# Kernel optimization log

Measured on AMD Instinct MI355X. Metric: run time of the kernel, lower is better.

The kernel has to match this reference:

```python
import jax, jax.numpy as jnp
import numpy as np

B, T, V, E, H, D = 2, 2048, 32000, 1024, 16, 64


def setup_inputs() -> dict:
    key = jax.random.key(0)
    ks = jax.random.split(key, 8)
    s = 0.02  # init scale
    return {
        "X": jax.random.randint(ks[0], (B, T), 0, V),
        "tok_emb": jax.random.normal(ks[1], (V, E), jnp.float32) * s,
        "pos_emb": jax.random.normal(ks[2], (T, E), jnp.float32) * s,
        "Wq": jax.random.normal(ks[3], (H, E, D), jnp.float32) * s,
        "Wk": jax.random.normal(ks[4], (H, E, D), jnp.float32) * s,
        "Wv": jax.random.normal(ks[5], (H, E, D), jnp.float32) * s,
        "lm_W": jax.random.normal(ks[6], (E, V), jnp.float32) * s,
        "lm_b": jnp.zeros((V,), jnp.float32),
    }


def reference(X, tok_emb, pos_emb, Wq, Wk, Wv, lm_W, lm_b):
    b, t = X.shape
    d = Wq.shape[-1]
    # token + position embedding
    x = tok_emb[X] + pos_emb[:t]  # [B,T,E]
    # per-head projections (stacked heads)
    q = jnp.einsum("bte,hed->bhtd", x, Wq)
    k = jnp.einsum("bte,hed->bhtd", x, Wk)
    v = jnp.einsum("bte,hed->bhtd", x, Wv)
    # causal attention, scale = head_size**-0.5
    scores = jnp.einsum("bhtd,bhsd->bhts", q, k) * (d ** -0.5)  # [B,H,T,T]
    mask = jnp.tril(jnp.ones((t, t), bool))
    scores = jnp.where(mask, scores, -jnp.inf)
    wei = jax.nn.softmax(scores, axis=-1)
    out = jnp.einsum("bhts,bhsd->bhtd", wei, v)
    out = out.transpose(0, 2, 1, 3).reshape(b, t, -1)  # concat heads -> [B,T,H*D]
    logits = out @ lm_W + lm_b  # [B,T,V]
    return logits
```

## Files before the change

kernel.cpp:

```cpp
#include <hip/hip_runtime.h>
#include <hip/hip_bf16.h>
#include <cstdint>

#define TSEQ 2048
#define NB   2
#define NH   16
#define EDIM 1024
#define DDIM 64
#define VOC  32000
#define MROWS (NB*TSEQ)
#define QKVN  (3*EDIM)

typedef _Float16 f16x8 __attribute__((ext_vector_type(8)));
typedef float    f32x4 __attribute__((ext_vector_type(4)));
typedef unsigned short u16x4v __attribute__((ext_vector_type(4)));
typedef unsigned short u16x8v __attribute__((ext_vector_type(8)));

__device__ __forceinline__ unsigned short f2h_bits(float v) {
  return __builtin_bit_cast(unsigned short, (_Float16)v);
}

__device__ __forceinline__ void gload_lds16(const void* g, void* l) {
  __builtin_amdgcn_global_load_lds((__attribute__((address_space(1))) void*)(g),
                                   (__attribute__((address_space(3))) void*)(l),
                                   16, 0, 0);
}

__global__ __launch_bounds__(256) void embed_kernel(
    const int* __restrict__ X, const float* __restrict__ tokE,
    const float* __restrict__ posE, unsigned short* __restrict__ x) {
  int g = blockIdx.x * 256 + threadIdx.x;
  int row = g >> 7;
  int e8  = (g & 127) * 8;
  int tk  = X[row];
  int tp  = row & (TSEQ - 1);
  const float4* ta = reinterpret_cast<const float4*>(&tokE[(size_t)tk * EDIM + e8]);
  const float4* pa = reinterpret_cast<const float4*>(&posE[(size_t)tp * EDIM + e8]);
  float4 a0 = ta[0], a1 = ta[1], p0 = pa[0], p1 = pa[1];
  u16x8v o;
  o[0] = f2h_bits(a0.x + p0.x); o[1] = f2h_bits(a0.y + p0.y);
  o[2] = f2h_bits(a0.z + p0.z); o[3] = f2h_bits(a0.w + p0.w);
  o[4] = f2h_bits(a1.x + p1.x); o[5] = f2h_bits(a1.y + p1.y);
  o[6] = f2h_bits(a1.z + p1.z); o[7] = f2h_bits(a1.w + p1.w);
  *reinterpret_cast<u16x8v*>(&x[(size_t)row * EDIM + e8]) = o;
}

__global__ __launch_bounds__(256) void trans_qkvw(
    const float* __restrict__ Wq, const float* __restrict__ Wk,
    const float* __restrict__ Wv, unsigned short* __restrict__ Wt) {
  __shared__ float ts[64][65];
  int bid = blockIdx.x;
  int mat = bid >> 8;
  int h   = (bid >> 4) & 15;
  int et  = bid & 15;
  const float* src = (mat == 0 ? Wq : (mat == 1 ? Wk : Wv)) + (size_t)h * EDIM * DDIM;
  int t = threadIdx.x;
  int rr = t >> 4, c4 = (t & 15) * 4;
#pragma unroll
  for (int p = 0; p < 4; ++p) {
    int r = p * 16 + rr;
    float4 v = *reinterpret_cast<const float4*>(&src[(size_t)(et * 64 + r) * DDIM + c4]);
    ts[r][c4 + 0] = v.x; ts[r][c4 + 1] = v.y; ts[r][c4 + 2] = v.z; ts[r][c4 + 3] = v.w;
  }
  __syncthreads();
#pragma unroll
  for (int p = 0; p < 4; ++p) {
    int dr = p * 16 + rr;
    u16x4v o;
#pragma unroll
    for (int j = 0; j < 4; ++j) o[j] = f2h_bits(ts[c4 + j][dr]);
    *reinterpret_cast<u16x4v*>(&Wt[((size_t)(mat * EDIM + h * 64 + dr)) * EDIM + et * 64 + c4]) = o;
  }
}

__global__ __launch_bounds__(256) void trans_lmw(
    const float* __restrict__ W, unsigned short* __restrict__ Wt) {
  __shared__ float ts[64][65];
  int bid = blockIdx.x;
  int vt = bid / 16, et = bid % 16;
  int t = threadIdx.x;
  int rr = t >> 4, c4 = (t & 15) * 4;
#pragma unroll
  for (int p = 0; p < 4; ++p) {
    int r = p * 16 + rr;
    float4 v = *reinterpret_cast<const float4*>(&W[(size_t)(et * 64 + r) * VOC + vt * 64 + c4]);
    ts[r][c4 + 0] = v.x; ts[r][c4 + 1] = v.y; ts[r][c4 + 2] = v.z; ts[r][c4 + 3] = v.w;
  }
  __syncthreads();
#pragma unroll
  for (int p = 0; p < 4; ++p) {
    int vr = p * 16 + rr;
    u16x4v o;
#pragma unroll
    for (int j = 0; j < 4; ++j) o[j] = f2h_bits(ts[c4 + j][vr]);
    *reinterpret_cast<u16x4v*>(&Wt[(size_t)(vt * 64 + vr) * EDIM + et * 64 + c4]) = o;
  }
}

template <bool F32OUT, bool BIAS>
__global__ __launch_bounds__(512, 4) void gemm128(
    const unsigned short* __restrict__ A, const unsigned short* __restrict__ Bt,
    float* __restrict__ Cf, unsigned short* __restrict__ Ch,
    const float* __restrict__ bias, int N, int K) {
  __shared__ __align__(16) unsigned short lds[3 * 12288];
  const int tid = threadIdx.x;
  const int w = tid >> 6, l = tid & 63;
  const int wr = w >> 2, wc = w & 3;
  const int l15 = l & 15, lhi = l >> 4;

  const int orig = blockIdx.x;
  const int bx = orig >> 5;
  const int by = orig & 31;
  const int m0 = by * 128, n0 = bx * 256;

  const int swzc = lhi ^ ((l15 >> 1) & 3);
  const int aOff = (wr * 64 + l15) * 32 + swzc * 8;
  const int bOff = 4096 + (wc * 64 + l15) * 32 + swzc * 8;

  const int sr = l >> 2;
  const int sc = (l & 3) ^ ((l >> 3) & 3);
  const unsigned short* PA = A  + (size_t)(m0 + w * 16 + sr) * K + sc * 8;
  const unsigned short* PB = Bt + (size_t)(n0 + w * 16 + sr) * K + sc * 8;
  const int dOff = w * 512;

#define STAGE32(ts, slot) do {                                                \
    gload_lds16(PA + (size_t)(ts) * 32, &lds[(slot) * 12288 + dOff]);         \
    gload_lds16(PB + (size_t)(ts) * 32, &lds[(slot) * 12288 + 4096 + dOff]);  \
    gload_lds16(PB + (size_t)128 * K + (size_t)(ts) * 32,                     \
                &lds[(slot) * 12288 + 8192 + dOff]);                          \
  } while (0)

  f32x4 acc[4][4] = {};
  STAGE32(0, 0);
  STAGE32(1, 1);
  asm volatile("s_waitcnt vmcnt(3)" ::: "memory");
  __builtin_amdgcn_sched_barrier(0);
  __builtin_amdgcn_s_barrier();

  const int NT = K >> 5;
  int slotC = 0;
  for (int t = 0; t < NT; ++t) {
    const int base = slotC * 12288;
    const int ts = (t + 2 < NT) ? (t + 2) : (NT - 1);
    int dslot = slotC + 2; if (dslot >= 3) dslot -= 3;
    STAGE32(ts, dslot);
    f16x8 af[4], bf[4];
#pragma unroll
    for (int q = 0; q < 4; ++q) af[q] = *reinterpret_cast<const f16x8*>(&lds[base + aOff + q * 512]);
#pragma unroll
    for (int q = 0; q < 4; ++q) bf[q] = *reinterpret_cast<const f16x8*>(&lds[base + bOff + q * 512]);
    asm volatile("s_waitcnt lgkmcnt(0)" ::: "memory");
    __builtin_amdgcn_sched_barrier(0);
    __builtin_amdgcn_s_setprio(1);
#pragma unroll
    for (int mi = 0; mi < 4; ++mi)
#pragma unroll
      for (int ni = 0; ni < 4; ++ni)
        acc[mi][ni] = __builtin_amdgcn_mfma_f32_16x16x32_f16(af[mi], bf[ni], acc[mi][ni], 0, 0, 0);
    __builtin_amdgcn_s_setprio(0);
    asm volatile("s_waitcnt vmcnt(3)" ::: "memory");
    __builtin_amdgcn_sched_barrier(0);
    __builtin_amdgcn_s_barrier();
    ++slotC; if (slotC == 3) slotC = 0;
  }
#undef STAGE32
  asm volatile("s_waitcnt vmcnt(0)" ::: "memory");

#pragma unroll
  for (int ni = 0; ni < 4; ++ni) {
    const int col = n0 + wc * 64 + ni * 16 + l15;
    float bv = BIAS ? bias[col] : 0.0f;
#pragma unroll
    for (int mi = 0; mi < 4; ++mi) {
#pragma unroll
      for (int r = 0; r < 4; ++r) {
        const size_t row = (size_t)m0 + wr * 64 + mi * 16 + lhi * 4 + r;
        float v = acc[mi][ni][r] + bv;
        if constexpr (F32OUT) __builtin_nontemporal_store(v, &Cf[row * (size_t)N + col]);
        else                  Ch[row * (size_t)N + col] = f2h_bits(v);
      }
    }
  }
}

__global__ __launch_bounds__(256) void attn_kernel(
    const unsigned short* __restrict__ qkv, unsigned short* __restrict__ out) {
  __shared__ unsigned short Vt[2][64 * 72];
  __shared__ unsigned short Pl[4 * 16 * 72];
  const int bid = blockIdx.x;
  const int qt = bid & 31, bh = bid >> 5;
  const int b = bh >> 4, h = bh & 15;
  const int tid = threadIdx.x, w = tid >> 6, l = tid & 63;
  const int l15 = l & 15, lhi = l >> 4;
  const int q0 = qt * 64;
  const size_t RS = QKVN;
  const unsigned short* qbase = qkv + (size_t)b * TSEQ * RS + h * 64;
  const unsigned short* kbase = qbase + EDIM;
  const unsigned short* vbase = qbase + 2 * EDIM;

  f16x8 qa[2];
  {
    const int qrow = q0 + w * 16 + l15;
#pragma unroll
    for (int ks = 0; ks < 2; ++ks)
      qa[ks] = *reinterpret_cast<const f16x8*>(qbase + (size_t)qrow * RS + ks * 32 + lhi * 8);
  }
  const int vr_ = tid >> 3, vc8 = (tid & 7) * 8;
  {
#pragma unroll
    for (int p = 0; p < 2; ++p) {
      const int rr = vr_ + p * 32;
      u16x8v v = *reinterpret_cast<const u16x8v*>(vbase + (size_t)rr * RS + vc8);
#pragma unroll
      for (int j = 0; j < 8; ++j) Vt[0][(vc8 + j) * 72 + rr] = v[j];
    }
  }
  float m_run[4], l_run[4];
  f32x4 o[4] = {};
#pragma unroll
  for (int r = 0; r < 4; ++r) { m_run[r] = -__builtin_inff(); l_run[r] = 0.f; }
  const int myrow = q0 + w * 16 + lhi * 4;
  unsigned short* pl = &Pl[w * 16 * 72];
  __syncthreads();

  for (int kt = 0; kt <= qt; ++kt) {
    const int kv0 = kt * 64;
    const int tn = (kt + 1 <= qt) ? (kt + 1) : qt;
    u16x8v vpre[2];
#pragma unroll
    for (int p = 0; p < 2; ++p)
      vpre[p] = *reinterpret_cast<const u16x8v*>(
          vbase + (size_t)(tn * 64 + vr_ + p * 32) * RS + vc8);
    f32x4 s[4];
    __builtin_amdgcn_s_setprio(1);
#pragma unroll
    for (int ct = 0; ct < 4; ++ct) {
      f32x4 acc = {};
#pragma unroll
      for (int ks = 0; ks < 2; ++ks) {
        f16x8 kb = *reinterpret_cast<const f16x8*>(
            kbase + (size_t)(kv0 + ct * 16 + l15) * RS + ks * 32 + lhi * 8);
        acc = __builtin_amdgcn_mfma_f32_16x16x32_f16(qa[ks], kb, acc, 0, 0, 0);
      }
      s[ct] = acc;
    }
    __builtin_amdgcn_s_setprio(0);
    if (kt == qt) {
#pragma unroll
      for (int ct = 0; ct < 4; ++ct) {
        const int col = kv0 + ct * 16 + l15;
#pragma unroll
        for (int r = 0; r < 4; ++r) {
          float v = s[ct][r] * 0.125f;
          if (col > myrow + r) v = -__builtin_inff();
          s[ct][r] = v;
        }
      }
    } else {
#pragma unroll
      for (int ct = 0; ct < 4; ++ct)
#pragma unroll
        for (int r = 0; r < 4; ++r) s[ct][r] *= 0.125f;
    }
    float alpha[4];
#pragma unroll
    for (int r = 0; r < 4; ++r) {
      float mx = fmaxf(fmaxf(s[0][r], s[1][r]), fmaxf(s[2][r], s[3][r]));
      mx = fmaxf(mx, __shfl_xor(mx, 1)); mx = fmaxf(mx, __shfl_xor(mx, 2));
      mx = fmaxf(mx, __shfl_xor(mx, 4)); mx = fmaxf(mx, __shfl_xor(mx, 8));
      const float mn = fmaxf(m_run[r], mx);
      alpha[r] = __expf(m_run[r] - mn);
      m_run[r] = mn;
    }
    float rs[4] = {0.f, 0.f, 0.f, 0.f};
#pragma unroll
    for (int ct = 0; ct < 4; ++ct)
#pragma unroll
      for (int r = 0; r < 4; ++r) {
        const float p = __expf(s[ct][r] - m_run[r]);
        s[ct][r] = p;
        rs[r] += p;
      }
#pragma unroll
    for (int r = 0; r < 4; ++r) {
      float t = rs[r];
      t += __shfl_xor(t, 1); t += __shfl_xor(t, 2);
      t += __shfl_xor(t, 4); t += __shfl_xor(t, 8);
      l_run[r] = l_run[r] * alpha[r] + t;
    }
#pragma unroll
    for (int ct = 0; ct < 4; ++ct)
#pragma unroll
      for (int r = 0; r < 4; ++r) o[ct][r] *= alpha[r];
#pragma unroll
    for (int ct = 0; ct < 4; ++ct)
#pragma unroll
      for (int r = 0; r < 4; ++r)
        pl[(lhi * 4 + r) * 72 + ct * 16 + l15] = f2h_bits(s[ct][r]);
    const unsigned short* vt = Vt[kt & 1];
#pragma unroll
    for (int ks = 0; ks < 2; ++ks) {
      f16x8 pa = *reinterpret_cast<const f16x8*>(&pl[l15 * 72 + ks * 32 + lhi * 8]);
      __builtin_amdgcn_s_setprio(1);
#pragma unroll
      for (int ct = 0; ct < 4; ++ct) {
        f16x8 vb = *reinterpret_cast<const f16x8*>(&vt[(ct * 16 + l15) * 72 + ks * 32 + lhi * 8]);
        o[ct] = __builtin_amdgcn_mfma_f32_16x16x32_f16(pa, vb, o[ct], 0, 0, 0);
      }
      __builtin_amdgcn_s_setprio(0);
    }
    if (kt < qt) {
      unsigned short* vtn = Vt[(kt + 1) & 1];
#pragma unroll
      for (int p = 0; p < 2; ++p) {
        const int rr = vr_ + p * 32;
#pragma unroll
        for (int j = 0; j < 8; ++j) vtn[(vc8 + j) * 72 + rr] = vpre[p][j];
      }
    }
    __syncthreads();
  }
  unsigned short* obase = out + ((size_t)(b * TSEQ + q0 + w * 16)) * EDIM + h * 64;
#pragma unroll
  for (int r = 0; r < 4; ++r) {
    const float linv = 1.0f / l_run[r];
#pragma unroll
    for (int ct = 0; ct < 4; ++ct) {
      obase[(size_t)(lhi * 4 + r) * EDIM + ct * 16 + l15] = f2h_bits(o[ct][r] * linv);
    }
  }
}

extern "C" void kernel_launch(void* const* d_in, const int* in_sizes, int n_in,
                              void* d_out, int out_size, void* d_ws, size_t ws_size,
                              hipStream_t stream) {
  const int*   X    = (const int*)d_in[0];
  const float* tokE = (const float*)d_in[1];
  const float* posE = (const float*)d_in[2];
  const float* Wq   = (const float*)d_in[3];
  const float* Wk   = (const float*)d_in[4];
  const float* Wv   = (const float*)d_in[5];
  const float* lmW  = (const float*)d_in[6];
  const float* lmb  = (const float*)d_in[7];
  float* out = (float*)d_out;

  unsigned short* ws   = (unsigned short*)d_ws;
  unsigned short* x    = ws;
  unsigned short* att  = x    + (size_t)MROWS * EDIM;
  unsigned short* wqkv = att  + (size_t)MROWS * EDIM;
  unsigned short* qkv  = wqkv + (size_t)QKVN * EDIM;
  unsigned short* lmWt = qkv  + (size_t)MROWS * QKVN;

  embed_kernel<<<(MROWS * EDIM / 8) / 256, 256, 0, stream>>>(X, tokE, posE, x);
  trans_qkvw<<<3 * NH * (EDIM / 64), 256, 0, stream>>>(Wq, Wk, Wv, wqkv);
  trans_lmw<<<(VOC / 64) * (EDIM / 64), 256, 0, stream>>>(lmW, lmWt);
  gemm128<false, false><<<(QKVN / 256) * (MROWS / 128), 512, 0, stream>>>(
      x, wqkv, nullptr, qkv, nullptr, QKVN, EDIM);
  attn_kernel<<<NB * NH * (TSEQ / 64), 256, 0, stream>>>(qkv, att);
  gemm128<true, true><<<(VOC / 256) * (MROWS / 128), 512, 0, stream>>>(
      att, lmWt, out, nullptr, lmb, VOC, EDIM);
}
```

Measured before the change: 559.6 us.

## Use 4-wave GEMM with larger per-wave tiles, reverse attention tile order, use exp2

The 128x256 GEMM now runs with 4 waves instead of 8. Each wave computes 128x64, so it holds twice the accumulators, and A fragments are prefetched one step ahead from LDS rather than waiting on all LDS reads first. Attention launches the longest causal query tiles first and folds log2(e) into the scale so it can use exp2f. The GEMM change raises MFMA work per LDS read but lowers occupancy and increases register pressure.

```diff
diff --git a/kernel.cpp b/kernel.cpp
--- a/kernel.cpp
+++ b/kernel.cpp
@@ -98,42 +98,46 @@
 }
 
 template <bool F32OUT, bool BIAS>
-__global__ __launch_bounds__(512, 4) void gemm128(
+__global__ __launch_bounds__(256, 2) void gemm128w(
     const unsigned short* __restrict__ A, const unsigned short* __restrict__ Bt,
     float* __restrict__ Cf, unsigned short* __restrict__ Ch,
     const float* __restrict__ bias, int N, int K) {
   __shared__ __align__(16) unsigned short lds[3 * 12288];
   const int tid = threadIdx.x;
   const int w = tid >> 6, l = tid & 63;
-  const int wr = w >> 2, wc = w & 3;
   const int l15 = l & 15, lhi = l >> 4;
-
   const int orig = blockIdx.x;
   const int bx = orig >> 5;
   const int by = orig & 31;
   const int m0 = by * 128, n0 = bx * 256;
 
   const int swzc = lhi ^ ((l15 >> 1) & 3);
-  const int aOff = (wr * 64 + l15) * 32 + swzc * 8;
-  const int bOff = 4096 + (wc * 64 + l15) * 32 + swzc * 8;
+  const int aOff = l15 * 32 + swzc * 8;
+  const int bOff = 4096 + (w * 64 + l15) * 32 + swzc * 8;
 
   const int sr = l >> 2;
   const int sc = (l & 3) ^ ((l >> 3) & 3);
   const unsigned short* PA = A  + (size_t)(m0 + w * 16 + sr) * K + sc * 8;
-  const unsigned short* PB = Bt + (size_t)(n0 + w * 16 + sr) * K + sc * 8;
-  const int dOff = w * 512;
-
-#define STAGE32(ts, slot) do {                                                \
-    gload_lds16(PA + (size_t)(ts) * 32, &lds[(slot) * 12288 + dOff]);         \
-    gload_lds16(PB + (size_t)(ts) * 32, &lds[(slot) * 12288 + 4096 + dOff]);  \
-    gload_lds16(PB + (size_t)128 * K + (size_t)(ts) * 32,                     \
-                &lds[(slot) * 12288 + 8192 + dOff]);                          \
+  const unsigned short* PB = Bt + (size_t)(n0 + w * 64 + sr) * K + sc * 8;
+
+#define STAGEW(ts, slot) do {                                                      \
+    gload_lds16(PA + (size_t)(ts) * 32, &lds[(slot) * 12288 + w * 512]);           \
+    gload_lds16(PA + (size_t)64 * K + (size_t)(ts) * 32,                           \
+                &lds[(slot) * 12288 + 2048 + w * 512]);                            \
+    gload_lds16(PB + (size_t)(ts) * 32,                                            \
+                &lds[(slot) * 12288 + 4096 + w * 2048]);                           \
+    gload_lds16(PB + (size_t)16 * K + (size_t)(ts) * 32,                           \
+                &lds[(slot) * 12288 + 4096 + w * 2048 + 512]);                     \
+    gload_lds16(PB + (size_t)32 * K + (size_t)(ts) * 32,                           \
+                &lds[(slot) * 12288 + 4096 + w * 2048 + 1024]);                    \
+    gload_lds16(PB + (size_t)48 * K + (size_t)(ts) * 32,                           \
+                &lds[(slot) * 12288 + 4096 + w * 2048 + 1536]);                    \
   } while (0)
 
-  f32x4 acc[4][4] = {};
-  STAGE32(0, 0);
-  STAGE32(1, 1);
-  asm volatile("s_waitcnt vmcnt(3)" ::: "memory");
+  f32x4 acc[8][4] = {};
+  STAGEW(0, 0);
+  STAGEW(1, 1);
+  asm volatile("s_waitcnt vmcnt(6)" ::: "memory");
   __builtin_amdgcn_sched_barrier(0);
   __builtin_amdgcn_s_barrier();
 
@@ -143,38 +147,38 @@
     const int base = slotC * 12288;
     const int ts = (t + 2 < NT) ? (t + 2) : (NT - 1);
     int dslot = slotC + 2; if (dslot >= 3) dslot -= 3;
-    STAGE32(ts, dslot);
-    f16x8 af[4], bf[4];
-#pragma unroll
-    for (int q = 0; q < 4; ++q) af[q] = *reinterpret_cast<const f16x8*>(&lds[base + aOff + q * 512]);
+    STAGEW(ts, dslot);
+    f16x8 bf[4];
 #pragma unroll
     for (int q = 0; q < 4; ++q) bf[q] = *reinterpret_cast<const f16x8*>(&lds[base + bOff + q * 512]);
-    asm volatile("s_waitcnt lgkmcnt(0)" ::: "memory");
-    __builtin_amdgcn_sched_barrier(0);
+    f16x8 afq = *reinterpret_cast<const f16x8*>(&lds[base + aOff]);
     __builtin_amdgcn_s_setprio(1);
 #pragma unroll
-    for (int mi = 0; mi < 4; ++mi)
+    for (int mi = 0; mi < 8; ++mi) {
+      f16x8 afn = *reinterpret_cast<const f16x8*>(&lds[base + aOff + (((mi + 1) & 7)) * 512]);
 #pragma unroll
       for (int ni = 0; ni < 4; ++ni)
-        acc[mi][ni] = __builtin_amdgcn_mfma_f32_16x16x32_f16(af[mi], bf[ni], acc[mi][ni], 0, 0, 0);
+        acc[mi][ni] = __builtin_amdgcn_mfma_f32_16x16x32_f16(afq, bf[ni], acc[mi][ni], 0, 0, 0);
+      afq = afn;
+    }
     __builtin_amdgcn_s_setprio(0);
-    asm volatile("s_waitcnt vmcnt(3)" ::: "memory");
+    asm volatile("s_waitcnt vmcnt(6)" ::: "memory");
     __builtin_amdgcn_sched_barrier(0);
     __builtin_amdgcn_s_barrier();
     ++slotC; if (slotC == 3) slotC = 0;
   }
-#undef STAGE32
+#undef STAGEW
   asm volatile("s_waitcnt vmcnt(0)" ::: "memory");
 
 #pragma unroll
   for (int ni = 0; ni < 4; ++ni) {
-    const int col = n0 + wc * 64 + ni * 16 + l15;
+    const int col = n0 + w * 64 + ni * 16 + l15;
     float bv = BIAS ? bias[col] : 0.0f;
 #pragma unroll
-    for (int mi = 0; mi < 4; ++mi) {
+    for (int mi = 0; mi < 8; ++mi) {
 #pragma unroll
       for (int r = 0; r < 4; ++r) {
-        const size_t row = (size_t)m0 + wr * 64 + mi * 16 + lhi * 4 + r;
+        const size_t row = (size_t)m0 + mi * 16 + lhi * 4 + r;
         float v = acc[mi][ni][r] + bv;
         if constexpr (F32OUT) __builtin_nontemporal_store(v, &Cf[row * (size_t)N + col]);
         else                  Ch[row * (size_t)N + col] = f2h_bits(v);
@@ -188,11 +192,13 @@
   __shared__ unsigned short Vt[2][64 * 72];
   __shared__ unsigned short Pl[4 * 16 * 72];
   const int bid = blockIdx.x;
-  const int qt = bid & 31, bh = bid >> 5;
+  const int qt = 31 - (bid & 31);
+  const int bh = bid >> 5;
   const int b = bh >> 4, h = bh & 15;
   const int tid = threadIdx.x, w = tid >> 6, l = tid & 63;
   const int l15 = l & 15, lhi = l >> 4;
   const int q0 = qt * 64;
+  const float SC = 0.125f * 1.44269504f;
   const size_t RS = QKVN;
   const unsigned short* qbase = qkv + (size_t)b * TSEQ * RS + h * 64;
   const unsigned short* kbase = qbase + EDIM;
@@ -251,7 +257,7 @@
         const int col = kv0 + ct * 16 + l15;
 #pragma unroll
         for (int r = 0; r < 4; ++r) {
-          float v = s[ct][r] * 0.125f;
+          float v = s[ct][r] * SC;
           if (col > myrow + r) v = -__builtin_inff();
           s[ct][r] = v;
         }
@@ -260,7 +266,7 @@
 #pragma unroll
       for (int ct = 0; ct < 4; ++ct)
 #pragma unroll
-        for (int r = 0; r < 4; ++r) s[ct][r] *= 0.125f;
+        for (int r = 0; r < 4; ++r) s[ct][r] *= SC;
     }
     float alpha[4];
 #pragma unroll
@@ -269,7 +275,7 @@
       mx = fmaxf(mx, __shfl_xor(mx, 1)); mx = fmaxf(mx, __shfl_xor(mx, 2));
       mx = fmaxf(mx, __shfl_xor(mx, 4)); mx = fmaxf(mx, __shfl_xor(mx, 8));
       const float mn = fmaxf(m_run[r], mx);
-      alpha[r] = __expf(m_run[r] - mn);
+      alpha[r] = exp2f(m_run[r] - mn);
       m_run[r] = mn;
     }
     float rs[4] = {0.f, 0.f, 0.f, 0.f};
@@ -277,7 +283,7 @@
     for (int ct = 0; ct < 4; ++ct)
 #pragma unroll
       for (int r = 0; r < 4; ++r) {
-        const float p = __expf(s[ct][r] - m_run[r]);
+        const float p = exp2f(s[ct][r] - m_run[r]);
         s[ct][r] = p;
         rs[r] += p;
       }
@@ -354,9 +360,9 @@
   embed_kernel<<<(MROWS * EDIM / 8) / 256, 256, 0, stream>>>(X, tokE, posE, x);
   trans_qkvw<<<3 * NH * (EDIM / 64), 256, 0, stream>>>(Wq, Wk, Wv, wqkv);
   trans_lmw<<<(VOC / 64) * (EDIM / 64), 256, 0, stream>>>(lmW, lmWt);
-  gemm128<false, false><<<(QKVN / 256) * (MROWS / 128), 512, 0, stream>>>(
+  gemm128w<false, false><<<(QKVN / 256) * (MROWS / 128), 256, 0, stream>>>(
       x, wqkv, nullptr, qkv, nullptr, QKVN, EDIM);
   attn_kernel<<<NB * NH * (TSEQ / 64), 256, 0, stream>>>(qkv, att);
-  gemm128<true, true><<<(VOC / 256) * (MROWS / 128), 512, 0, stream>>>(
+  gemm128w<true, true><<<(VOC / 256) * (MROWS / 128), 256, 0, stream>>>(
       att, lmWt, out, nullptr, lmb, VOC, EDIM);
 }
```

Result: faster. 535.7 us (-4.3%).
